# Optimization experiments

Hardware: AMD Instinct MI355X
Metric: run time of the kernel (lower is better)

The kernel has to match this reference:

```python
import jax, jax.numpy as jnp
import numpy as np

N_POS = 8192
BATCH = 4
N_GT = 512
EPS = 1e-6
P_EXP = -1.0  # generalized-mean exponent (p < 0)


def setup_inputs() -> dict:
    key = jax.random.key(0)
    k1, k2, k3 = jax.random.split(key, 3)
    dis_matrix = jax.random.uniform(k1, (N_POS, N_POS), dtype=jnp.float32)
    prob_map = jax.random.uniform(k2, (BATCH, N_POS), dtype=jnp.float32)
    gt = jax.random.randint(k3, (BATCH, N_GT), 0, N_POS, dtype=jnp.int64 if jax.config.jax_enable_x64 else jnp.int32)
    return {"prob_map": prob_map, "gt": gt, "dis_matrix": dis_matrix}


def reference(prob_map, gt, dis_matrix):
    max_dist = jnp.max(dis_matrix)
    # global min-max normalization with detached min/range (matches torch .detach())
    pmin = jax.lax.stop_gradient(jnp.min(prob_map))
    prange = jax.lax.stop_gradient(jnp.max(prob_map) - jnp.min(prob_map))
    prob = jnp.clip((prob_map - pmin) / prange, 0.0, 1.0)  # (B, N)

    # gather gt-indexed columns: dis_matrix[:, gt] -> (N, B, G) -> (B, N, G)
    D = jnp.transpose(jnp.take(dis_matrix, gt, axis=1), (1, 0, 2))

    n_est = prob.sum(axis=1)  # (B,)
    # term 1: (1/n_est) * sum_n p_n * min_g D[n, g]
    term1 = jnp.sum(prob * jnp.min(D, axis=2), axis=1) / (n_est + EPS)  # (B,)

    # term 2: generalized mean over pixel dim of weighted distance matrix
    w = (1.0 - prob)[:, :, None] * max_dist + prob[:, :, None] * D  # (B, N, G)
    minn = jnp.mean((w + EPS) ** P_EXP, axis=1) ** (1.0 / P_EXP)  # (B, G)
    term2 = jnp.mean(minn, axis=1)  # (B,)

    return jnp.mean(term1) + jnp.mean(term2)
```

## Files before the change

### kernel.cpp

```cpp
#include <hip/hip_runtime.h>
#include <math.h>

#define N_POS 8192
#define BATCH 4
#define N_GT 512
#define BG (BATCH * N_GT)
#define EPSV 1e-6f

#define WS_DPACK 0
#define WS_PARTS 16777216
#define WS_MIND  18874368
#define WS_PMAX  18907136
#define WS_SC    18908160

#define KA_BLOCKS 1024
#define ROWS_A 8
#define KC_BLOCKS 1024
#define ROWS_C 8

__global__ __launch_bounds__(256) void whd_kA(const float* __restrict__ dis,
                                              const int* __restrict__ gt,
                                              float* __restrict__ wsf) {
    __shared__ float rowbuf[N_POS];
    __shared__ unsigned short gtl[BG];
    __shared__ float minsh[4][4];
    __shared__ float smax[4];
    int t = threadIdx.x;
    int wv = t >> 6, lane = t & 63;
    int row0 = blockIdx.x * ROWS_A;
    float* dpack = wsf + WS_DPACK;
    float* minD = wsf + WS_MIND;

    for (int i = t; i < BG; i += 256) gtl[i] = (unsigned short)gt[i];
    __syncthreads();
    int c[8];
    #pragma unroll
    for (int k = 0; k < 8; k++) c[k] = gtl[t + 256 * k];

    float tmax = -INFINITY;
    for (int r = 0; r < ROWS_A; r++) {
        int n = row0 + r;
        if (r > 0) {
            __syncthreads();
            if (t < BATCH) {
                float m = fminf(fminf(minsh[0][t], minsh[1][t]), fminf(minsh[2][t], minsh[3][t]));
                minD[t * N_POS + (n - 1)] = m;
            }
        }
        const float4* src = (const float4*)(dis + (size_t)n * N_POS);
        float4* dstl = (float4*)rowbuf;
        #pragma unroll
        for (int j = 0; j < N_POS / 4 / 256; j++) {
            int i = t + 256 * j;
            float4 v = src[i];
            tmax = fmaxf(tmax, fmaxf(fmaxf(v.x, v.y), fmaxf(v.z, v.w)));
            dstl[i] = v;
        }
        __syncthreads();
        float vmin[4];
        #pragma unroll
        for (int k = 0; k < 8; k++) {
            float v = rowbuf[c[k]];
            dpack[(size_t)n * BG + t + 256 * k] = v;
            int b = k >> 1;
            if ((k & 1) == 0) vmin[b] = v; else vmin[b] = fminf(vmin[b], v);
        }
        #pragma unroll
        for (int b = 0; b < BATCH; b++) {
            float m = vmin[b];
            #pragma unroll
            for (int off = 32; off; off >>= 1) m = fminf(m, __shfl_xor(m, off, 64));
            if (lane == 0) minsh[wv][b] = m;
        }
    }
    __syncthreads();
    if (t < BATCH) {
        float m = fminf(fminf(minsh[0][t], minsh[1][t]), fminf(minsh[2][t], minsh[3][t]));
        minD[t * N_POS + (row0 + ROWS_A - 1)] = m;
    }
    #pragma unroll
    for (int off = 32; off; off >>= 1) tmax = fmaxf(tmax, __shfl_down(tmax, off, 64));
    if (lane == 0) smax[wv] = tmax;
    __syncthreads();
    if (t == 0)
        wsf[WS_PMAX + blockIdx.x] = fmaxf(fmaxf(smax[0], smax[1]), fmaxf(smax[2], smax[3]));
}

__global__ __launch_bounds__(1024) void whd_kB1(const float* __restrict__ prob,
                                                float* __restrict__ wsf) {
    __shared__ float red[1024];
    int t = threadIdx.x;
    float m = -INFINITY;
    for (int i = t; i < KA_BLOCKS; i += 1024) m = fmaxf(m, wsf[WS_PMAX + i]);
    red[t] = m; __syncthreads();
    for (int s = 512; s; s >>= 1) { if (t < s) red[t] = fmaxf(red[t], red[t + s]); __syncthreads(); }
    float maxdist = red[0]; __syncthreads();
    float lmin = INFINITY, lmax = -INFINITY;
    for (int i = t; i < BATCH * N_POS; i += 1024) {
        float v = prob[i];
        lmin = fminf(lmin, v); lmax = fmaxf(lmax, v);
    }
    red[t] = lmin; __syncthreads();
    for (int s = 512; s; s >>= 1) { if (t < s) red[t] = fminf(red[t], red[t + s]); __syncthreads(); }
    float pmin = red[0]; __syncthreads();
    red[t] = lmax; __syncthreads();
    for (int s = 512; s; s >>= 1) { if (t < s) red[t] = fmaxf(red[t], red[t + s]); __syncthreads(); }
    float pmax = red[0];
    if (t == 0) {
        wsf[WS_SC + 0] = maxdist;
        wsf[WS_SC + 1] = pmin;
        wsf[WS_SC + 2] = pmax - pmin;
    }
    if (t >= 3 && t < 12) wsf[WS_SC + t] = 0.f;
}

__global__ __launch_bounds__(128) void whd_kB2(const float* __restrict__ prob,
                                               float* __restrict__ wsf) {
    __shared__ float sred[2];
    int t = threadIdx.x;
    int n = blockIdx.x * 128 + t;
    float pmin = wsf[WS_SC + 1];
    float invr = 1.0f / wsf[WS_SC + 2];
    const float* minD = wsf + WS_MIND;
    #pragma unroll
    for (int b = 0; b < BATCH; b++) {
        float p = (prob[b * N_POS + n] - pmin) * invr;
        p = fminf(fmaxf(p, 0.f), 1.f);
        float pm = p * minD[b * N_POS + n];
        #pragma unroll
        for (int off = 32; off; off >>= 1) {
            p += __shfl_down(p, off, 64);
            pm += __shfl_down(pm, off, 64);
        }
        if ((t & 63) == 0) { if (t == 64) { sred[0] = p; sred[1] = pm; } }
        __syncthreads();
        if (t == 0) {
            atomicAdd(&wsf[WS_SC + 3 + b], p + sred[0]);
            atomicAdd(&wsf[WS_SC + 7 + b], pm + sred[1]);
        }
        __syncthreads();
    }
}

__global__ __launch_bounds__(256) void whd_kC(const float* __restrict__ prob,
                                              float* __restrict__ wsf) {
    int t = threadIdx.x;
    int row0 = blockIdx.x * ROWS_C;
    const float* dpack = wsf + WS_DPACK;
    float maxd = wsf[WS_SC + 0];
    float pmin = wsf[WS_SC + 1];
    float invr = 1.0f / wsf[WS_SC + 2];
    float acc[8];
    #pragma unroll
    for (int k = 0; k < 8; k++) acc[k] = 0.f;
    for (int r = 0; r < ROWS_C; r++) {
        int n = row0 + r;
        float pb[4];
        #pragma unroll
        for (int b = 0; b < BATCH; b++) {
            float p = (prob[b * N_POS + n] - pmin) * invr;
            pb[b] = fminf(fmaxf(p, 0.f), 1.f);
        }
        const float* rowp = dpack + (size_t)n * BG;
        #pragma unroll
        for (int k = 0; k < 8; k++) {
            float d = rowp[t + 256 * k];
            float w = fmaf(pb[k >> 1], d - maxd, maxd) + EPSV;
            acc[k] += 1.0f / w;
        }
    }
    float* outp = wsf + WS_PARTS + (size_t)blockIdx.x * BG;
    #pragma unroll
    for (int k = 0; k < 8; k++) outp[t + 256 * k] = acc[k];
}

__global__ __launch_bounds__(256) void whd_kD(float* __restrict__ wsf) {
    __shared__ float red[256];
    int t = threadIdx.x;
    int col = blockIdx.x * 256 + t;
    const float* parts = wsf + WS_PARTS;
    float s = 0.f;
    for (int ch = 0; ch < KC_BLOCKS; ch++) s += parts[(size_t)ch * BG + col];
    float val = (float)N_POS / s;
    red[t] = val; __syncthreads();
    for (int st = 128; st; st >>= 1) { if (t < st) red[t] += red[t + st]; __syncthreads(); }
    if (t == 0) atomicAdd(&wsf[WS_SC + 11], red[0]);
}

__global__ __launch_bounds__(64) void whd_kE(const float* __restrict__ wsf,
                                             float* __restrict__ out) {
    if (threadIdx.x == 0) {
        float term1 = 0.f;
        for (int b = 0; b < BATCH; b++)
            term1 += wsf[WS_SC + 7 + b] / (wsf[WS_SC + 3 + b] + EPSV);
        term1 *= (1.0f / BATCH);
        float term2 = wsf[WS_SC + 11] * (1.0f / BG);
        out[0] = term1 + term2;
    }
}

extern "C" void kernel_launch(void* const* d_in, const int* in_sizes, int n_in,
                              void* d_out, int out_size, void* d_ws, size_t ws_size,
                              hipStream_t stream) {
    const float* prob = (const float*)d_in[0];
    const int* gt = (const int*)d_in[1];
    const float* dis = (const float*)d_in[2];
    float* out = (float*)d_out;
    float* wsf = (float*)d_ws;

    whd_kA<<<KA_BLOCKS, 256, 0, stream>>>(dis, gt, wsf);
    whd_kB1<<<1, 1024, 0, stream>>>(prob, wsf);
    whd_kB2<<<N_POS / 128, 128, 0, stream>>>(prob, wsf);
    whd_kC<<<KC_BLOCKS, 256, 0, stream>>>(prob, wsf);
    whd_kD<<<BG / 256, 256, 0, stream>>>(wsf);
    whd_kE<<<1, 64, 0, stream>>>(wsf, out);
}
```

Baseline: 472.5 us.

## Map one wave per batch, vectorize packed stores, merge B kernels, halve rows per block

Gathered columns are now assigned so each thread owns 8 consecutive gt entries, and each wave owns one batch. This lets the packed matrix be written and read as float4 pairs, and the per-batch min becomes a single wave shuffle reduction instead of a cross-wave shared-memory step. The two prob-statistics kernels are merged into one single-block kernel, which removes one launch and the atomics but runs the whole reduction in one block. Rows per block drop from 8 to 4, doubling the block count and doubling the partial-sum buffer that kD has to reduce.

Result: slower. 574.8 us (+21.6%).

```diff
diff --git a/kernel.cpp b/kernel.cpp
--- a/kernel.cpp
+++ b/kernel.cpp
@@ -4,30 +4,29 @@
 #define N_POS 8192
 #define BATCH 4
 #define N_GT 512
-#define BG (BATCH * N_GT)
+#define BG 2048
 #define EPSV 1e-6f
 
+#define KA_BLOCKS 2048
+#define ROWS_A 4
+#define KC_BLOCKS 2048
+#define ROWS_C 4
+
 #define WS_DPACK 0
-#define WS_PARTS 16777216
-#define WS_MIND  18874368
-#define WS_PMAX  18907136
-#define WS_SC    18908160
-
-#define KA_BLOCKS 1024
-#define ROWS_A 8
-#define KC_BLOCKS 1024
-#define ROWS_C 8
+#define WS_PARTS (N_POS * BG)
+#define WS_MIND  (WS_PARTS + KC_BLOCKS * BG)
+#define WS_MAXP  (WS_MIND + BATCH * N_POS)
+#define WS_SC    (WS_MAXP + KA_BLOCKS)
 
 __global__ __launch_bounds__(256) void whd_kA(const float* __restrict__ dis,
                                               const int* __restrict__ gt,
                                               float* __restrict__ wsf) {
     __shared__ float rowbuf[N_POS];
     __shared__ unsigned short gtl[BG];
-    __shared__ float minsh[4][4];
     __shared__ float smax[4];
-    int t = threadIdx.x;
-    int wv = t >> 6, lane = t & 63;
-    int row0 = blockIdx.x * ROWS_A;
+    const int t = threadIdx.x;
+    const int wv = t >> 6, lane = t & 63;
+    const int row0 = blockIdx.x * ROWS_A;
     float* dpack = wsf + WS_DPACK;
     float* minD = wsf + WS_MIND;
 
@@ -35,18 +34,12 @@
     __syncthreads();
     int c[8];
     #pragma unroll
-    for (int k = 0; k < 8; k++) c[k] = gtl[t + 256 * k];
+    for (int k = 0; k < 8; k++) c[k] = gtl[8 * t + k];
 
     float tmax = -INFINITY;
     for (int r = 0; r < ROWS_A; r++) {
-        int n = row0 + r;
-        if (r > 0) {
-            __syncthreads();
-            if (t < BATCH) {
-                float m = fminf(fminf(minsh[0][t], minsh[1][t]), fminf(minsh[2][t], minsh[3][t]));
-                minD[t * N_POS + (n - 1)] = m;
-            }
-        }
+        const int n = row0 + r;
+        if (r > 0) __syncthreads();
         const float4* src = (const float4*)(dis + (size_t)n * N_POS);
         float4* dstl = (float4*)rowbuf;
         #pragma unroll
@@ -57,41 +50,31 @@
             dstl[i] = v;
         }
         __syncthreads();
-        float vmin[4];
+        float g0 = rowbuf[c[0]], g1 = rowbuf[c[1]], g2 = rowbuf[c[2]], g3 = rowbuf[c[3]];
+        float g4 = rowbuf[c[4]], g5 = rowbuf[c[5]], g6 = rowbuf[c[6]], g7 = rowbuf[c[7]];
+        float4* dst = (float4*)(dpack + (size_t)n * BG + 8 * t);
+        dst[0] = make_float4(g0, g1, g2, g3);
+        dst[1] = make_float4(g4, g5, g6, g7);
+        float m = fminf(fminf(fminf(g0, g1), fminf(g2, g3)),
+                        fminf(fminf(g4, g5), fminf(g6, g7)));
         #pragma unroll
-        for (int k = 0; k < 8; k++) {
-            float v = rowbuf[c[k]];
-            dpack[(size_t)n * BG + t + 256 * k] = v;
-            int b = k >> 1;
-            if ((k & 1) == 0) vmin[b] = v; else vmin[b] = fminf(vmin[b], v);
-        }
-        #pragma unroll
-        for (int b = 0; b < BATCH; b++) {
-            float m = vmin[b];
-            #pragma unroll
-            for (int off = 32; off; off >>= 1) m = fminf(m, __shfl_xor(m, off, 64));
-            if (lane == 0) minsh[wv][b] = m;
-        }
-    }
-    __syncthreads();
-    if (t < BATCH) {
-        float m = fminf(fminf(minsh[0][t], minsh[1][t]), fminf(minsh[2][t], minsh[3][t]));
-        minD[t * N_POS + (row0 + ROWS_A - 1)] = m;
+        for (int off = 32; off; off >>= 1) m = fminf(m, __shfl_xor(m, off, 64));
+        if (lane == 0) minD[wv * N_POS + n] = m;
     }
     #pragma unroll
     for (int off = 32; off; off >>= 1) tmax = fmaxf(tmax, __shfl_down(tmax, off, 64));
     if (lane == 0) smax[wv] = tmax;
     __syncthreads();
     if (t == 0)
-        wsf[WS_PMAX + blockIdx.x] = fmaxf(fmaxf(smax[0], smax[1]), fmaxf(smax[2], smax[3]));
+        wsf[WS_MAXP + blockIdx.x] = fmaxf(fmaxf(smax[0], smax[1]), fmaxf(smax[2], smax[3]));
 }
 
-__global__ __launch_bounds__(1024) void whd_kB1(const float* __restrict__ prob,
-                                                float* __restrict__ wsf) {
+__global__ __launch_bounds__(1024) void whd_kB(const float* __restrict__ prob,
+                                               float* __restrict__ wsf) {
     __shared__ float red[1024];
-    int t = threadIdx.x;
+    const int t = threadIdx.x;
     float m = -INFINITY;
-    for (int i = t; i < KA_BLOCKS; i += 1024) m = fmaxf(m, wsf[WS_PMAX + i]);
+    for (int i = t; i < KA_BLOCKS; i += 1024) m = fmaxf(m, wsf[WS_MAXP + i]);
     red[t] = m; __syncthreads();
     for (int s = 512; s; s >>= 1) { if (t < s) red[t] = fmaxf(red[t], red[t + s]); __syncthreads(); }
     float maxdist = red[0]; __syncthreads();
@@ -105,81 +88,74 @@
     float pmin = red[0]; __syncthreads();
     red[t] = lmax; __syncthreads();
     for (int s = 512; s; s >>= 1) { if (t < s) red[t] = fmaxf(red[t], red[t + s]); __syncthreads(); }
-    float pmax = red[0];
+    float pmax = red[0]; __syncthreads();
+    float invr = 1.0f / (pmax - pmin);
+    const float* minD = wsf + WS_MIND;
+    for (int b = 0; b < BATCH; b++) {
+        float sp = 0.f, spm = 0.f;
+        for (int i = t; i < N_POS; i += 1024) {
+            float p = (prob[b * N_POS + i] - pmin) * invr;
+            p = fminf(fmaxf(p, 0.f), 1.f);
+            sp += p;
+            spm += p * minD[b * N_POS + i];
+        }
+        red[t] = sp; __syncthreads();
+        for (int s = 512; s; s >>= 1) { if (t < s) red[t] += red[t + s]; __syncthreads(); }
+        if (t == 0) wsf[WS_SC + 3 + b] = red[0];
+        __syncthreads();
+        red[t] = spm; __syncthreads();
+        for (int s = 512; s; s >>= 1) { if (t < s) red[t] += red[t + s]; __syncthreads(); }
+        if (t == 0) wsf[WS_SC + 7 + b] = red[0];
+        __syncthreads();
+    }
     if (t == 0) {
         wsf[WS_SC + 0] = maxdist;
         wsf[WS_SC + 1] = pmin;
         wsf[WS_SC + 2] = pmax - pmin;
-    }
-    if (t >= 3 && t < 12) wsf[WS_SC + t] = 0.f;
-}
-
-__global__ __launch_bounds__(128) void whd_kB2(const float* __restrict__ prob,
-                                               float* __restrict__ wsf) {
-    __shared__ float sred[2];
-    int t = threadIdx.x;
-    int n = blockIdx.x * 128 + t;
-    float pmin = wsf[WS_SC + 1];
-    float invr = 1.0f / wsf[WS_SC + 2];
-    const float* minD = wsf + WS_MIND;
-    #pragma unroll
-    for (int b = 0; b < BATCH; b++) {
-        float p = (prob[b * N_POS + n] - pmin) * invr;
-        p = fminf(fmaxf(p, 0.f), 1.f);
-        float pm = p * minD[b * N_POS + n];
-        #pragma unroll
-        for (int off = 32; off; off >>= 1) {
-            p += __shfl_down(p, off, 64);
-            pm += __shfl_down(pm, off, 64);
-        }
-        if ((t & 63) == 0) { if (t == 64) { sred[0] = p; sred[1] = pm; } }
-        __syncthreads();
-        if (t == 0) {
-            atomicAdd(&wsf[WS_SC + 3 + b], p + sred[0]);
-            atomicAdd(&wsf[WS_SC + 7 + b], pm + sred[1]);
-        }
-        __syncthreads();
+        wsf[WS_SC + 11] = 0.f;
     }
 }
 
 __global__ __launch_bounds__(256) void whd_kC(const float* __restrict__ prob,
                                               float* __restrict__ wsf) {
-    int t = threadIdx.x;
-    int row0 = blockIdx.x * ROWS_C;
+    const int t = threadIdx.x;
+    const int wv = t >> 6;
+    const int row0 = blockIdx.x * ROWS_C;
     const float* dpack = wsf + WS_DPACK;
-    float maxd = wsf[WS_SC + 0];
-    float pmin = wsf[WS_SC + 1];
-    float invr = 1.0f / wsf[WS_SC + 2];
+    const float maxd = wsf[WS_SC + 0];
+    const float pmin = wsf[WS_SC + 1];
+    const float invr = 1.0f / wsf[WS_SC + 2];
     float acc[8];
     #pragma unroll
     for (int k = 0; k < 8; k++) acc[k] = 0.f;
+    #pragma unroll
     for (int r = 0; r < ROWS_C; r++) {
-        int n = row0 + r;
-        float pb[4];
-        #pragma unroll
-        for (int b = 0; b < BATCH; b++) {
-            float p = (prob[b * N_POS + n] - pmin) * invr;
-            pb[b] = fminf(fmaxf(p, 0.f), 1.f);
-        }
-        const float* rowp = dpack + (size_t)n * BG;
-        #pragma unroll
-        for (int k = 0; k < 8; k++) {
-            float d = rowp[t + 256 * k];
-            float w = fmaf(pb[k >> 1], d - maxd, maxd) + EPSV;
-            acc[k] += 1.0f / w;
-        }
+        const int n = row0 + r;
+        float p = (prob[wv * N_POS + n] - pmin) * invr;
+        p = fminf(fmaxf(p, 0.f), 1.f);
+        const float4* rp = (const float4*)(dpack + (size_t)n * BG + 8 * t);
+        float4 v0 = rp[0], v1 = rp[1];
+        acc[0] += 1.0f / (fmaf(p, v0.x - maxd, maxd) + EPSV);
+        acc[1] += 1.0f / (fmaf(p, v0.y - maxd, maxd) + EPSV);
+        acc[2] += 1.0f / (fmaf(p, v0.z - maxd, maxd) + EPSV);
+        acc[3] += 1.0f / (fmaf(p, v0.w - maxd, maxd) + EPSV);
+        acc[4] += 1.0f / (fmaf(p, v1.x - maxd, maxd) + EPSV);
+        acc[5] += 1.0f / (fmaf(p, v1.y - maxd, maxd) + EPSV);
+        acc[6] += 1.0f / (fmaf(p, v1.z - maxd, maxd) + EPSV);
+        acc[7] += 1.0f / (fmaf(p, v1.w - maxd, maxd) + EPSV);
     }
-    float* outp = wsf + WS_PARTS + (size_t)blockIdx.x * BG;
-    #pragma unroll
-    for (int k = 0; k < 8; k++) outp[t + 256 * k] = acc[k];
+    float4* op = (float4*)(wsf + WS_PARTS + (size_t)blockIdx.x * BG + 8 * t);
+    op[0] = make_float4(acc[0], acc[1], acc[2], acc[3]);
+    op[1] = make_float4(acc[4], acc[5], acc[6], acc[7]);
 }
 
 __global__ __launch_bounds__(256) void whd_kD(float* __restrict__ wsf) {
     __shared__ float red[256];
-    int t = threadIdx.x;
-    int col = blockIdx.x * 256 + t;
+    const int t = threadIdx.x;
+    const int col = blockIdx.x * 256 + t;
     const float* parts = wsf + WS_PARTS;
     float s = 0.f;
+    #pragma unroll 8
     for (int ch = 0; ch < KC_BLOCKS; ch++) s += parts[(size_t)ch * BG + col];
     float val = (float)N_POS / s;
     red[t] = val; __syncthreads();
@@ -209,8 +185,7 @@
     float* wsf = (float*)d_ws;
 
     whd_kA<<<KA_BLOCKS, 256, 0, stream>>>(dis, gt, wsf);
-    whd_kB1<<<1, 1024, 0, stream>>>(prob, wsf);
-    whd_kB2<<<N_POS / 128, 128, 0, stream>>>(prob, wsf);
+    whd_kB<<<1, 1024, 0, stream>>>(prob, wsf);
     whd_kC<<<KC_BLOCKS, 256, 0, stream>>>(prob, wsf);
     whd_kD<<<BG / 256, 256, 0, stream>>>(wsf);
     whd_kE<<<1, 64, 0, stream>>>(wsf, out);
```
